# Optimization experiments

Hardware: AMD Instinct MI355X
Metric: run time of the kernel (lower is better)

The kernel has to match this reference:

```python
import jax, jax.numpy as jnp
import numpy as np

B, T, EPROJS, DUNITS, ATT_DIM, ODIM, LMAX = 16, 800, 512, 1024, 512, 5000, 96
SOS = EOS = ODIM - 1
SCALING = 2.0  # ESPnet AttAdd default softmax scaling


def setup_inputs() -> dict:
    key = jax.random.key(0)
    ks = jax.random.split(key, 16)
    w = lambda i, shape: (jax.random.normal(ks[i], shape, jnp.float32) * 0.02)
    return {
        "hs_pad": jax.random.normal(ks[0], (B, T, EPROJS), jnp.float32),
        "hlens": jnp.full((B,), T, dtype=jnp.int32),
        "ys_pad": jax.random.randint(ks[1], (B, LMAX), 0, ODIM - 2, dtype=jnp.int32),
        "embed": w(2, (ODIM, DUNITS)),
        # layer 0 LSTMCell: input = [embed ; att_context]
        "W_ih0": w(3, (4 * DUNITS, DUNITS + EPROJS)),
        "W_hh0": w(4, (4 * DUNITS, DUNITS)),
        "b_ih0": jnp.zeros((4 * DUNITS,), jnp.float32),
        "b_hh0": jnp.zeros((4 * DUNITS,), jnp.float32),
        # layer 1 LSTMCell
        "W_ih1": w(5, (4 * DUNITS, DUNITS)),
        "W_hh1": w(6, (4 * DUNITS, DUNITS)),
        "b_ih1": jnp.zeros((4 * DUNITS,), jnp.float32),
        "b_hh1": jnp.zeros((4 * DUNITS,), jnp.float32),
        # AttAdd (additive attention)
        "W_enc": w(7, (ATT_DIM, EPROJS)),
        "b_enc": jnp.zeros((ATT_DIM,), jnp.float32),
        "W_dec": w(8, (ATT_DIM, DUNITS)),
        "gvec": w(9, (ATT_DIM,)),
        # output projection (context_residual=False -> dunits -> odim)
        "W_out": w(10, (ODIM, DUNITS)),
        "b_out": jnp.zeros((ODIM,), jnp.float32),
    }


def _lstm_cell(x, h, c, W_ih, W_hh, b_ih, b_hh):
    g = x @ W_ih.T + b_ih + h @ W_hh.T + b_hh  # (B, 4D), torch gate order i,f,g,o
    i, f, gg, o = jnp.split(g, 4, axis=-1)
    c_new = jax.nn.sigmoid(f) * c + jax.nn.sigmoid(i) * jnp.tanh(gg)
    h_new = jax.nn.sigmoid(o) * jnp.tanh(c_new)
    return h_new, c_new


def reference(hs_pad, hlens, ys_pad, embed, W_ih0, W_hh0, b_ih0, b_hh0,
              W_ih1, W_hh1, b_ih1, b_hh1, W_enc, b_enc, W_dec, gvec,
              W_out, b_out):
    batch = ys_pad.shape[0]
    # ys_in = [sos; y], ys_out = [y; eos]  (all targets full length -> no ignore_id)
    sos_col = jnp.full((batch, 1), SOS, dtype=ys_pad.dtype)
    eos_col = jnp.full((batch, 1), EOS, dtype=ys_pad.dtype)
    ys_in = jnp.concatenate([sos_col, ys_pad], axis=1)   # (B, L+1)
    ys_out = jnp.concatenate([ys_pad, eos_col], axis=1)  # (B, L+1)
    olength = ys_out.shape[1]

    eys = embed[ys_in]  # (B, L+1, D)  dropout_emb is identity (p=0)

    # precompute encoder projection for additive attention (done once, as in ESPnet)
    pre_enc = jnp.einsum('bte,ae->bta', hs_pad, W_enc) + b_enc  # (B, T, ATT)
    mask = jnp.arange(hs_pad.shape[1])[None, :] < hlens[:, None]  # (B, T)

    z0 = jnp.zeros((batch, DUNITS), hs_pad.dtype)
    zeros = (z0, z0, z0, z0)  # z0, c0, z1, c1

    def step(carry, ey_t):
        z0, c0, z1, c1 = carry
        # AttAdd: e = gvec . tanh(W_enc h + W_dec z0)
        dec_proj = z0 @ W_dec.T  # (B, ATT)
        e = jnp.tanh(pre_enc + dec_proj[:, None, :]) @ gvec  # (B, T)
        e = jnp.where(mask, e, -jnp.inf)
        att_w = jax.nn.softmax(SCALING * e, axis=-1)
        att_c = jnp.einsum('bt,bte->be', att_w, hs_pad)  # (B, EPROJS)
        x = jnp.concatenate([ey_t, att_c], axis=-1)  # (B, D+EPROJS)
        z0, c0 = _lstm_cell(x, z0, c0, W_ih0, W_hh0, b_ih0, b_hh0)
        z1, c1 = _lstm_cell(z0, z1, c1, W_ih1, W_hh1, b_ih1, b_hh1)
        return (z0, c0, z1, c1), z1

    _, z_all = jax.lax.scan(step, zeros, jnp.swapaxes(eys, 0, 1))  # (L+1, B, D)
    z_all = jnp.swapaxes(z_all, 0, 1)  # (B, L+1, D)

    logits = jnp.einsum('bld,od->blo', z_all, W_out) + b_out  # (B, L+1, ODIM)
    logp = jax.nn.log_softmax(logits, axis=-1)
    nll = -jnp.take_along_axis(logp, ys_out[..., None].astype(jnp.int32), axis=-1)[..., 0]
    loss = jnp.mean(nll)  # reduction='mean' over all tokens (no ignored targets)
    # ESPnet: self.loss *= (mean(len(ys_in)) - 1) = LMAX
    loss = loss * jnp.asarray(LMAX, loss.dtype)
    return loss
```

## Files before the change

kernel.cpp:

```cpp
#include <hip/hip_runtime.h>
#include <stdint.h>

#define Bsz 16
#define Tlen 800
#define EPROJS 512
#define DUNITS 1024
#define ATT 512
#define ODIM 5000
#define LMAX 96
#define OL 97
#define NTOK (OL*Bsz)
#define G4 (4*DUNITS)
#define KX 1536
#define KA1 2048
#define SOS_ID (ODIM-1)
#define NWG 512
#define TCH 25

typedef unsigned short u16;
typedef unsigned int u32;
typedef unsigned long long u64;
typedef short bfrag8 __attribute__((ext_vector_type(8)));
typedef float f32x4 __attribute__((ext_vector_type(4)));

__device__ __forceinline__ float bf2f(u16 u){
  union { uint32_t u; float f; } v; v.u = ((uint32_t)u) << 16; return v.f;
}
__device__ __forceinline__ u16 f2bf(float f){
  union { float f; uint32_t u; } v; v.f = f;
  uint32_t r = v.u + 0x7FFFu + ((v.u >> 16) & 1u);
  return (u16)(r >> 16);
}
__device__ __forceinline__ float sigm(float x){ return 1.0f/(1.0f + __expf(-x)); }
__device__ __forceinline__ float tanh_f(float x){ return 1.0f - 2.0f/(__expf(2.0f*x) + 1.0f); }

__device__ __forceinline__ u64 ald64(const void* p){
  return __hip_atomic_load((const u64*)p, __ATOMIC_RELAXED, __HIP_MEMORY_SCOPE_AGENT);
}
__device__ __forceinline__ void ast64(void* p, u64 v){
  __hip_atomic_store((u64*)p, v, __ATOMIC_RELAXED, __HIP_MEMORY_SCOPE_AGENT);
}
__device__ __forceinline__ float aldf(const float* p){
  return __hip_atomic_load(p, __ATOMIC_RELAXED, __HIP_MEMORY_SCOPE_AGENT);
}
__device__ __forceinline__ void astf(float* p, float v){
  __hip_atomic_store(p, v, __ATOMIC_RELAXED, __HIP_MEMORY_SCOPE_AGENT);
}
__device__ __forceinline__ void ast32(u32* p, u32 v){
  __hip_atomic_store(p, v, __ATOMIC_RELAXED, __HIP_MEMORY_SCOPE_AGENT);
}
__device__ __forceinline__ int ald32(const int* p){
  return __hip_atomic_load(p, __ATOMIC_RELAXED, __HIP_MEMORY_SCOPE_AGENT);
}
__device__ __forceinline__ bfrag8 aldfrag(const u16* p){
  union { u64 q[2]; bfrag8 f; } u;
  u.q[0] = ald64(p);
  u.q[1] = ald64(p + 4);
  return u.f;
}

__device__ __forceinline__ f32x4 mfma_loop_a(const u16* A, int lda,
                                             const u16* Bm, int ldb,
                                             int K, f32x4 acc){
  int lane = threadIdx.x & 63;
  const u16* pa = A + (size_t)(lane & 15) * lda + ((lane >> 4) * 8);
  const u16* pb = Bm + (size_t)(lane & 15) * ldb + ((lane >> 4) * 8);
  #pragma unroll 4
  for (int k = 0; k < K; k += 32){
    bfrag8 av = aldfrag(pa + k);
    bfrag8 bv = *(const bfrag8*)(pb + k);
    acc = __builtin_amdgcn_mfma_f32_16x16x32_bf16(av, bv, acc, 0, 0, 0);
  }
  return acc;
}
__device__ __forceinline__ f32x4 mfma_loop(const u16* A, int lda,
                                           const u16* Bm, int ldb,
                                           int K, f32x4 acc){
  int lane = threadIdx.x & 63;
  const u16* pa = A + (size_t)(lane & 15) * lda + ((lane >> 4) * 8);
  const u16* pb = Bm + (size_t)(lane & 15) * ldb + ((lane >> 4) * 8);
  #pragma unroll 4
  for (int k = 0; k < K; k += 32){
    bfrag8 av = *(const bfrag8*)(pa + k);
    bfrag8 bv = *(const bfrag8*)(pb + k);
    acc = __builtin_amdgcn_mfma_f32_16x16x32_bf16(av, bv, acc, 0, 0, 0);
  }
  return acc;
}

__device__ __forceinline__ void wait_slots(const u64* s64, int n64, int tgt){
  __syncthreads();
  if (threadIdx.x < 64){
    int ln = threadIdx.x;
    bool d0 = (ln >= n64), d1 = (ln + 64 >= n64);
    for(;;){
      if (!d0){ u64 v = ald64(&s64[ln]);
        d0 = ((int)(u32)v >= tgt) && ((int)(u32)(v >> 32) >= tgt); }
      if (!d1){ u64 v = ald64(&s64[ln + 64]);
        d1 = ((int)(u32)v >= tgt) && ((int)(u32)(v >> 32) >= tgt); }
      if (__all(d0 && d1)) break;
      __builtin_amdgcn_s_sleep(1);
    }
  }
  __syncthreads();
}
__device__ __forceinline__ void signal_slot(int* slot, int val){
  __syncthreads();
  if (threadIdx.x == 0) ast32((u32*)slot, (u32)val);
}

__global__ __launch_bounds__(256) void k_zero(float* p, int n){
  int i = blockIdx.x*256 + threadIdx.x;
  if (i < n) p[i] = 0.f;
}
__global__ __launch_bounds__(256) void k_cvt(const float* src, u16* dst, int n){
  int i = blockIdx.x*256 + threadIdx.x, st = gridDim.x*256;
  for (; i < n; i += st) dst[i] = f2bf(src[i]);
}
__global__ __launch_bounds__(256) void k_build_wc0p(const float* Whh0, const float* Wih0, u16* out){
  int i = blockIdx.x*256+threadIdx.x, n = 256*16*KX, st = gridDim.x*256;
  for (; i<n; i+=st){
    int k = i % KX, ws = i / KX;
    int s = ws & 15, w2 = ws >> 4;
    int r = (s>>2)*1024 + 4*w2 + (s&3);
    float v = (k < 1024) ? Whh0[(size_t)r*1024 + k] : Wih0[(size_t)r*KX + k];
    out[i] = f2bf(v);
  }
}
__global__ __launch_bounds__(256) void k_build_wc1p(const float* Wih1, const float* Whh1, u16* out){
  int i = blockIdx.x*256+threadIdx.x, n = 256*16*KA1, st = gridDim.x*256;
  for (; i<n; i+=st){
    int k = i % KA1, ws = i / KA1;
    int s = ws & 15, w2 = ws >> 4;
    int r = (s>>2)*1024 + 4*w2 + (s&3);
    float v = (k < 1024) ? Wih1[(size_t)r*1024 + k] : Whh1[(size_t)r*1024 + (k-1024)];
    out[i] = f2bf(v);
  }
}
__global__ __launch_bounds__(256) void k_build_wih0p(const float* Wih0, u16* out){
  int i = blockIdx.x*256+threadIdx.x, n = 256*16*DUNITS, st = gridDim.x*256;
  for (; i<n; i+=st){
    int k = i % DUNITS, ws = i / DUNITS;
    int s = ws & 15, w2 = ws >> 4;
    int r = (s>>2)*1024 + 4*w2 + (s&3);
    out[i] = f2bf(Wih0[(size_t)r*KX + k]);
  }
}
__global__ __launch_bounds__(256) void k_build_aey(const float* embed, const int* ys_pad, u16* out){
  int i = blockIdx.x*256+threadIdx.x, n = NTOK*DUNITS, st = gridDim.x*256;
  for (; i<n; i+=st){
    int row = i / DUNITS, k = i % DUNITS;
    int l = row / Bsz, b = row % Bsz;
    int idx = (l == 0) ? SOS_ID : ys_pad[b*LMAX + (l-1)];
    out[i] = f2bf(embed[(size_t)idx*DUNITS + k]);
  }
}

__global__ __launch_bounds__(64) void k_gemm_preenc(const u16* hsb, const u16* Wenc,
                                                    const float* b_enc, u16* pre_enc){
  int bid = blockIdx.x;
  int m0 = (bid >> 5) * 16, n0 = (bid & 31) * 16;
  int lane = threadIdx.x & 63;
  int col = n0 + (lane & 15);
  float bias = b_enc[col];
  f32x4 acc = {bias, bias, bias, bias};
  acc = mfma_loop(hsb + (size_t)m0*EPROJS, EPROJS, Wenc + (size_t)n0*EPROJS, EPROJS, EPROJS, acc);
  int quad = lane >> 4;
  #pragma unroll
  for (int r = 0; r < 4; r++)
    pre_enc[(size_t)(m0 + quad*4 + r)*ATT + col] = f2bf(acc[r]);
}

__global__ __launch_bounds__(64) void k_gemm_logits(const u16* zall, const u16* Woutb,
                                                    const float* b_out, float* logits){
  const int NT = 313;
  int bid = blockIdx.x;
  int m0 = (bid / NT) * 16, n0 = (bid % NT) * 16;
  int lane = threadIdx.x & 63;
  int col = n0 + (lane & 15);
  bool ok = col < ODIM;
  int brow = ok ? col : 0;
  float bias = ok ? b_out[col] : 0.f;
  f32x4 acc = {bias, bias, bias, bias};
  const u16* pa = zall + (size_t)m0*DUNITS + (size_t)(lane & 15)*DUNITS + (lane >> 4)*8;
  const u16* pb = Woutb + (size_t)brow*DUNITS + (lane >> 4)*8;
  #pragma unroll 4
  for (int k = 0; k < DUNITS; k += 32){
    bfrag8 av = *(const bfrag8*)(pa + k);
    bfrag8 bv = *(const bfrag8*)(pb + k);
    acc = __builtin_amdgcn_mfma_f32_16x16x32_bf16(av, bv, acc, 0, 0, 0);
  }
  int quad = lane >> 4;
  if (ok){
    #pragma unroll
    for (int r = 0; r < 4; r++)
      logits[(size_t)(m0 + quad*4 + r)*ODIM + col] = acc[r];
  }
}

__global__ __launch_bounds__(256) void k_nll(const float* logits, const int* ys_pad, float* nll){
  int n = blockIdx.x;
  int b = n & 15, l = n >> 4;
  const float* row = logits + (size_t)n * ODIM;
  __shared__ float red[256];
  float m = -1e30f;
  for (int i = threadIdx.x; i < ODIM; i += 256) m = fmaxf(m, row[i]);
  red[threadIdx.x] = m; __syncthreads();
  for (int s = 128; s > 0; s >>= 1){
    if (threadIdx.x < s) red[threadIdx.x] = fmaxf(red[threadIdx.x], red[threadIdx.x + s]);
    __syncthreads();
  }
  float M = red[0]; __syncthreads();
  float sum = 0.f;
  for (int i = threadIdx.x; i < ODIM; i += 256) sum += __expf(row[i] - M);
  red[threadIdx.x] = sum; __syncthreads();
  for (int s = 128; s > 0; s >>= 1){
    if (threadIdx.x < s) red[threadIdx.x] += red[threadIdx.x + s];
    __syncthreads();
  }
  if (threadIdx.x == 0){
    int tgt = (l < LMAX) ? ys_pad[b*LMAX + l] : (ODIM - 1);
    nll[n] = (M + __logf(red[0])) - row[tgt];
  }
}

__global__ __launch_bounds__(256) void k_loss(const float* nll, float* out){
  __shared__ float red[256];
  float s = 0.f;
  for (int i = threadIdx.x; i < NTOK; i += 256) s += nll[i];
  red[threadIdx.x] = s; __syncthreads();
  for (int st = 128; st > 0; st >>= 1){
    if (threadIdx.x < st) red[threadIdx.x] += red[threadIdx.x + st];
    __syncthreads();
  }
  if (threadIdx.x == 0) out[0] = red[0] * ((float)LMAX / (float)NTOK);
}

__global__ __launch_bounds__(256, 2) void k_persist(
  const u16* __restrict__ peb, const u16* __restrict__ hsb,
  const u16* __restrict__ wc0p, const u16* __restrict__ wc1p, const u16* __restrict__ wdecb,
  const u16* __restrict__ wih0p, const u16* __restrict__ aey,
  const float* __restrict__ b_ih0, const float* __restrict__ b_hh0,
  const float* __restrict__ b_ih1, const float* __restrict__ b_hh1,
  const float* __restrict__ gvec, const int* __restrict__ hlens,
  u16* a1b0, u16* a1b1, float* dpbuf, float* part, float* partS, u16* xatt,
  u16* zall, int* bar)
{
  __shared__ __align__(16) u16 s_pe[TCH*512];
  __shared__ __align__(16) u16 s_hs[TCH*512];
  __shared__ __align__(16) float s_dp[512];
  __shared__ __align__(16) float s_gv[512];
  __shared__ __align__(16) float s_red[2048];
  __shared__ float s_c[64];
  __shared__ float s_bias[16];
  __shared__ float s_bias0[16];
  __shared__ float s_sp[4];
  __shared__ __align__(8) u16 s_h[64];

  int tid = threadIdx.x, blk = blockIdx.x;
  int wv = tid >> 6, ln = tid & 63;
  int s2_b = blk >> 5, s2_ch = blk & 31;
  int t0 = s2_ch * TCH;
  int hl = hlens[s2_b];
  bool isLow = (blk < 256);
  int hw = blk - 256;
  bool isdp = (!isLow) && ((hw & 7) == 0);
  int wdp = hw >> 3;

  int* z0s  = bar;
  int* z1s  = bar + 256;
  int* dps  = bar + 512;
  int* atts = bar + 544;
  int* parts= bar + 576;

  {
    const bfrag8* src_pe = (const bfrag8*)(peb + ((size_t)(s2_b*Tlen + t0))*512);
    const bfrag8* src_hs = (const bfrag8*)(hsb + ((size_t)(s2_b*Tlen + t0))*512);
    for (int idx = tid; idx < TCH*512/8; idx += 256){
      ((bfrag8*)s_pe)[idx] = src_pe[idx];
      ((bfrag8*)s_hs)[idx] = src_hs[idx];
    }
    for (int a = tid; a < 512; a += 256) s_gv[a] = gvec[a];
    if (isLow && tid < 16){
      int r = (tid>>2)*1024 + 4*blk + (tid&3);
      s_bias[tid] = b_ih1[r] + b_hh1[r];
    }
    if (!isLow && tid < 16){
      int r = (tid>>2)*1024 + 4*hw + (tid&3);
      s_bias0[tid] = b_ih0[r] + b_hh0[r];
    }
    if (tid < 64) s_c[tid] = 0.f;
  }
  __syncthreads();

  for (int i = 0; i < OL; i++){
    int par = i & 1;
    const u16* a1r = par ? a1b1 : a1b0;
    u16* a1w = par ? a1b0 : a1b1;
    float* dpc   = dpbuf + (size_t)par*(16*512);
    float* partc = part  + (size_t)par*(16*32*512);
    float* pSc   = partS + (size_t)par*(16*32);
    u16*   xac   = xatt  + (size_t)par*(16*512);

    f32x4 acc0 = {0.f,0.f,0.f,0.f};

    if (!isLow){
      if (isdp){
        if (i >= 1) wait_slots((const u64*)z0s, 128, i);
        const u16* btd = wdecb + (size_t)wdp*16*DUNITS;
        f32x4 ad = {0.f,0.f,0.f,0.f};
        ad = mfma_loop_a(a1r + wv*256, KA1, btd + wv*256, DUNITS, 256, ad);
        int q = ln >> 4;
        #pragma unroll
        for (int r = 0; r < 4; r++) s_red[wv*256 + (q*4+r)*16 + (ln & 15)] = ad[r];
        __syncthreads();
        {
          float val = s_red[tid] + s_red[256+tid] + s_red[512+tid] + s_red[768+tid];
          int b = tid >> 4, al = tid & 15;
          astf(&dpc[b*512 + wdp*16 + al], val);
        }
        signal_slot(&dps[wdp], i + 1);
      }
      acc0 = mfma_loop(aey + ((size_t)i*Bsz)*DUNITS + wv*256, DUNITS,
                       wih0p + (size_t)hw*16*DUNITS + wv*256, DUNITS, 256, acc0);
    }

    wait_slots((const u64*)dps, 16, i + 1);
    ((u64*)s_dp)[tid] = ald64(((const u64*)(dpc + s2_b*512)) + tid);
    __syncthreads();
    {
      float dpr[8], gvr[8];
      {
        float4 d1 = *(const float4*)&s_dp[ln*8];
        float4 d2 = *(const float4*)&s_dp[ln*8+4];
        float4 g1 = *(const float4*)&s_gv[ln*8];
        float4 g2 = *(const float4*)&s_gv[ln*8+4];
        dpr[0]=d1.x; dpr[1]=d1.y; dpr[2]=d1.z; dpr[3]=d1.w;
        dpr[4]=d2.x; dpr[5]=d2.y; dpr[6]=d2.z; dpr[7]=d2.w;
        gvr[0]=g1.x; gvr[1]=g1.y; gvr[2]=g1.z; gvr[3]=g1.w;
        gvr[4]=g2.x; gvr[5]=g2.y; gvr[6]=g2.z; gvr[7]=g2.w;
      }
      float attc[8];
      #pragma unroll
      for (int j = 0; j < 8; j++) attc[j] = 0.f;
      float sp = 0.f;
      for (int lt = wv; lt < TCH; lt += 4){
        int t = t0 + lt;
        bool valid = (t < hl);
        float e = 0.f;
        if (valid){
          bfrag8 pv = *(const bfrag8*)&s_pe[lt*512 + ln*8];
          #pragma unroll
          for (int j = 0; j < 8; j++){
            float x = bf2f(((u16*)&pv)[j]) + dpr[j];
            e += gvr[j] * tanh_f(x);
          }
        }
        #pragma unroll
        for (int off = 32; off > 0; off >>= 1) e += __shfl_xor(e, off, 64);
        float p = valid ? __expf(2.0f * e) : 0.f;
        if (ln == 0) sp += p;
        bfrag8 hv = *(const bfrag8*)&s_hs[lt*512 + ln*8];
        #pragma unroll
        for (int j = 0; j < 8; j++) attc[j] += p * bf2f(((u16*)&hv)[j]);
      }
      *(float4*)&s_red[wv*512 + ln*8]     = make_float4(attc[0],attc[1],attc[2],attc[3]);
      *(float4*)&s_red[wv*512 + ln*8 + 4] = make_float4(attc[4],attc[5],attc[6],attc[7]);
      if (ln == 0) s_sp[wv] = sp;
      __syncthreads();
      {
        int e0 = 2*tid;
        float v0 = s_red[e0]   + s_red[512+e0]   + s_red[1024+e0]   + s_red[1536+e0];
        float v1 = s_red[e0+1] + s_red[512+e0+1] + s_red[1024+e0+1] + s_red[1536+e0+1];
        union { float f[2]; u64 q; } pu; pu.f[0]=v0; pu.f[1]=v1;
        ast64(&partc[((size_t)(s2_b*32 + s2_ch))*512 + e0], pu.q);
      }
      if (tid == 0) astf(&pSc[s2_b*32 + s2_ch], s_sp[0]+s_sp[1]+s_sp[2]+s_sp[3]);
      signal_slot(&parts[s2_b*32 + s2_ch], i + 1);
    }

    if (isLow){
      if (blk < 16 && wv == 0){
        const int* myparts = parts + blk*32;
        bool dn = (ln >= 32);
        for(;;){
          if (!dn) dn = (ald32(&myparts[ln]) >= i + 1);
          if (__all(dn)) break;
          __builtin_amdgcn_s_sleep(1);
        }
        float sp = (ln < 32) ? aldf(&pSc[blk*32 + ln]) : 0.f;
        #pragma unroll
        for (int off = 32; off > 0; off >>= 1) sp += __shfl_xor(sp, off, 64);
        float rinv = 1.0f / sp;
        float v0=0.f,v1=0.f,v2=0.f,v3=0.f,v4=0.f,v5=0.f,v6=0.f,v7=0.f;
        #pragma unroll 8
        for (int c2 = 0; c2 < 32; c2++){
          const u64* pp = (const u64*)(partc + ((size_t)(blk*32 + c2))*512) + ln*4;
          union { u64 q; float f[2]; } x0,x1,x2,x3;
          x0.q = ald64(pp); x1.q = ald64(pp+1);
          x2.q = ald64(pp+2); x3.q = ald64(pp+3);
          v0 += x0.f[0]; v1 += x0.f[1]; v2 += x1.f[0]; v3 += x1.f[1];
          v4 += x2.f[0]; v5 += x2.f[1]; v6 += x3.f[0]; v7 += x3.f[1];
        }
        u32 p0 = (u32)f2bf(v0*rinv) | ((u32)f2bf(v1*rinv) << 16);
        u32 p1 = (u32)f2bf(v2*rinv) | ((u32)f2bf(v3*rinv) << 16);
        u32 p2 = (u32)f2bf(v4*rinv) | ((u32)f2bf(v5*rinv) << 16);
        u32 p3 = (u32)f2bf(v6*rinv) | ((u32)f2bf(v7*rinv) << 16);
        ast64(&xac[blk*512 + ln*8],     ((u64)p1 << 32) | p0);
        ast64(&xac[blk*512 + ln*8 + 4], ((u64)p3 << 32) | p2);
        asm volatile("s_waitcnt vmcnt(0)" ::: "memory");
        if (ln == 0) ast32((u32*)&atts[blk], (u32)(i + 1));
      }
      if (i >= 1){
        if (i >= 2) wait_slots((const u64*)z1s, 128, i);
        const u16* bt = wc1p + (size_t)blk*16*KA1;
        f32x4 acc = {0.f,0.f,0.f,0.f};
        acc = mfma_loop_a(a1r + wv*512, KA1, bt + wv*512, KA1, 512, acc);
        int q = ln >> 4;
        #pragma unroll
        for (int r = 0; r < 4; r++) s_red[wv*256 + (q*4+r)*16 + (ln & 15)] = acc[r];
        __syncthreads();
        {
          float val = s_red[tid] + s_red[256+tid] + s_red[512+tid] + s_red[768+tid]
                    + s_bias[tid & 15];
          s_red[1024 + tid] = val;
        }
        __syncthreads();
        if (tid < 64){
          int b = tid >> 2, jj = tid & 3;
          float gi = s_red[1024 + b*16 + jj];
          float gf = s_red[1024 + b*16 + 4 + jj];
          float gg = s_red[1024 + b*16 + 8 + jj];
          float go = s_red[1024 + b*16 + 12 + jj];
          float c = s_c[tid];
          float cn = sigm(gf)*c + sigm(gi)*tanh_f(gg);
          float h  = sigm(go)*tanh_f(cn);
          s_c[tid] = cn;
          s_h[tid] = f2bf(h);
        }
        __syncthreads();
        if (tid < 16){
          u64 hq = ((u64*)s_h)[tid];
          ast64(&a1w[tid*KA1 + 1024 + 4*blk], hq);
          *(u64*)&zall[((size_t)(i-1)*Bsz + tid)*DUNITS + 4*blk] = hq;
        }
        signal_slot(&z1s[blk], i + 1);
      }
    } else {
      const u16* bt0 = wc0p + (size_t)hw*16*KX;
      acc0 = mfma_loop_a(a1r + wv*256, KA1, bt0 + wv*256, KX, 256, acc0);
      wait_slots((const u64*)atts, 8, i + 1);
      acc0 = mfma_loop_a(xac + wv*128, 512, bt0 + 1024 + wv*128, KX, 128, acc0);
      int q = ln >> 4;
      #pragma unroll
      for (int r = 0; r < 4; r++) s_red[wv*256 + (q*4+r)*16 + (ln & 15)] = acc0[r];
      __syncthreads();
      {
        float val = s_red[tid] + s_red[256+tid] + s_red[512+tid] + s_red[768+tid]
                  + s_bias0[tid & 15];
        s_red[1024 + tid] = val;
      }
      __syncthreads();
      if (tid < 64){
        int b = tid >> 2, jj = tid & 3;
        float gi = s_red[1024 + b*16 + jj];
        float gf = s_red[1024 + b*16 + 4 + jj];
        float gg = s_red[1024 + b*16 + 8 + jj];
        float go = s_red[1024 + b*16 + 12 + jj];
        float c = s_c[tid];
        float cn = sigm(gf)*c + sigm(gi)*tanh_f(gg);
        float h  = sigm(go)*tanh_f(cn);
        s_c[tid] = cn;
        s_h[tid] = f2bf(h);
      }
      __syncthreads();
      if (tid < 16) ast64(&a1w[tid*KA1 + 4*hw], ((u64*)s_h)[tid]);
      signal_slot(&z0s[hw], i + 1);
    }
  }

  if (isLow){
    wait_slots((const u64*)z0s, 128, OL);
    wait_slots((const u64*)z1s, 128, OL);
    const u16* a1r = (OL & 1) ? a1b1 : a1b0;
    const u16* bt = wc1p + (size_t)blk*16*KA1;
    f32x4 acc = {0.f,0.f,0.f,0.f};
    acc = mfma_loop_a(a1r + wv*512, KA1, bt + wv*512, KA1, 512, acc);
    int q = ln >> 4;
    #pragma unroll
    for (int r = 0; r < 4; r++) s_red[wv*256 + (q*4+r)*16 + (ln & 15)] = acc[r];
    __syncthreads();
    {
      float val = s_red[tid] + s_red[256+tid] + s_red[512+tid] + s_red[768+tid]
                + s_bias[tid & 15];
      s_red[1024 + tid] = val;
    }
    __syncthreads();
    if (tid < 64){
      int b = tid >> 2, jj = tid & 3;
      float gi = s_red[1024 + b*16 + jj];
      float gf = s_red[1024 + b*16 + 4 + jj];
      float gg = s_red[1024 + b*16 + 8 + jj];
      float go = s_red[1024 + b*16 + 12 + jj];
      float c = s_c[tid];
      float cn = sigm(gf)*c + sigm(gi)*tanh_f(gg);
      float h  = sigm(go)*tanh_f(cn);
      s_h[tid] = f2bf(h);
    }
    __syncthreads();
    if (tid < 16)
      *(u64*)&zall[((size_t)LMAX*Bsz + tid)*DUNITS + 4*blk] = ((u64*)s_h)[tid];
  }
}

extern "C" void kernel_launch(void* const* d_in, const int* in_sizes, int n_in,
                              void* d_out, int out_size, void* d_ws, size_t ws_size,
                              hipStream_t stream)
{
  const float* hs     = (const float*)d_in[0];
  const int*   hlens  = (const int*)d_in[1];
  const int*   ys_pad = (const int*)d_in[2];
  const float* embed  = (const float*)d_in[3];
  const float* W_ih0  = (const float*)d_in[4];
  const float* W_hh0  = (const float*)d_in[5];
  const float* b_ih0  = (const float*)d_in[6];
  const float* b_hh0  = (const float*)d_in[7];
  const float* W_ih1  = (const float*)d_in[8];
  const float* W_hh1  = (const float*)d_in[9];
  const float* b_ih1  = (const float*)d_in[10];
  const float* b_hh1  = (const float*)d_in[11];
  const float* W_enc  = (const float*)d_in[12];
  const float* b_enc  = (const float*)d_in[13];
  const float* W_dec  = (const float*)d_in[14];
  const float* gvec   = (const float*)d_in[15];
  const float* W_out  = (const float*)d_in[16];
  const float* b_out  = (const float*)d_in[17];
  (void)in_sizes; (void)n_in; (void)out_size; (void)ws_size;

  char* w = (char*)d_ws;
  size_t off = 0;
  auto alloc = [&](size_t bytes)->char*{
    char* ptr = w + off;
    off += (bytes + 255) & ~(size_t)255;
    return ptr;
  };
  int*   bar  = (int*)alloc(8192);
  u16*  a1b0  = (u16*)alloc(Bsz*KA1*2);
  u16*  a1b1  = (u16*)alloc(Bsz*KA1*2);
  size_t state_bytes = off;
  float* dpbuf = (float*)alloc(2*(size_t)Bsz*ATT*4);
  float* part  = (float*)alloc(2*(size_t)Bsz*32*512*4);
  float* partS = (float*)alloc(2*(size_t)Bsz*32*4);
  u16*  xatt   = (u16*)alloc(2*(size_t)Bsz*512*2);
  u16*  hsb    = (u16*)alloc((size_t)Bsz*Tlen*EPROJS*2);
  u16*  peb    = (u16*)alloc((size_t)Bsz*Tlen*ATT*2);
  u16*  wencb  = (u16*)alloc((size_t)ATT*EPROJS*2);
  u16*  wdecb  = (u16*)alloc((size_t)ATT*DUNITS*2);
  u16*  wc0p   = (u16*)alloc((size_t)G4*KX*2);
  u16*  wc1p   = (u16*)alloc((size_t)G4*KA1*2);
  u16*  wih0p  = (u16*)alloc((size_t)G4*DUNITS*2);
  u16*  woutb  = (u16*)alloc((size_t)ODIM*DUNITS*2);
  u16*  aey    = (u16*)alloc((size_t)NTOK*DUNITS*2);
  u16*  zall   = (u16*)alloc((size_t)NTOK*DUNITS*2);
  float* logits= (float*)alloc((size_t)NTOK*ODIM*4);
  float* nll   = (float*)alloc(NTOK*4);

  {
    int n = (int)(state_bytes / 4);
    k_zero<<<(n + 255)/256, 256, 0, stream>>>((float*)w, n);
  }

  k_cvt<<<2048,256,0,stream>>>(hs, hsb, Bsz*Tlen*EPROJS);
  k_cvt<<<256,256,0,stream>>>(W_enc, wencb, ATT*EPROJS);
  k_cvt<<<512,256,0,stream>>>(W_dec, wdecb, ATT*DUNITS);
  k_cvt<<<2048,256,0,stream>>>(W_out, woutb, ODIM*DUNITS);
  k_build_wc0p<<<4096,256,0,stream>>>(W_hh0, W_ih0, wc0p);
  k_build_wc1p<<<4096,256,0,stream>>>(W_ih1, W_hh1, wc1p);
  k_build_wih0p<<<4096,256,0,stream>>>(W_ih0, wih0p);
  k_build_aey<<<1024,256,0,stream>>>(embed, ys_pad, aey);

  k_gemm_preenc<<<(Bsz*Tlen/16)*(ATT/16), 64, 0, stream>>>(hsb, wencb, b_enc, peb);

  {
    void* args[] = {
      (void*)&peb, (void*)&hsb, (void*)&wc0p, (void*)&wc1p, (void*)&wdecb,
      (void*)&wih0p, (void*)&aey, (void*)&b_ih0, (void*)&b_hh0,
      (void*)&b_ih1, (void*)&b_hh1, (void*)&gvec, (void*)&hlens,
      (void*)&a1b0, (void*)&a1b1, (void*)&dpbuf, (void*)&part, (void*)&partS,
      (void*)&xatt, (void*)&zall, (void*)&bar
    };
    hipLaunchCooperativeKernel((const void*)k_persist, dim3(NWG), dim3(256),
                               args, 0, stream);
  }

  k_gemm_logits<<<OL*313, 64, 0, stream>>>(zall, woutb, b_out, logits);
  k_nll<<<NTOK,256,0,stream>>>(logits, ys_pad, nll);
  k_loss<<<1,256,0,stream>>>(nll, (float*)d_out);
}
```

Measured before the change: 3.357 ms.

## Replace per-block flag barriers with sharded atomic counters and last-arriver attention reduction

After: 3.624 ms. 8.0% more time.

```diff
diff --git a/kernel.cpp b/kernel.cpp
--- a/kernel.cpp
+++ b/kernel.cpp
@@ -88,25 +88,30 @@
   return acc;
 }
 
-__device__ __forceinline__ void wait_slots(const u64* s64, int n64, int tgt){
+__device__ __forceinline__ void wait_cnt1(const int* p, int tgt){
+  __syncthreads();
+  if (threadIdx.x == 0){
+    while (ald32(p) < tgt) __builtin_amdgcn_s_sleep(1);
+  }
+  __syncthreads();
+}
+__device__ __forceinline__ void wait_cnt8(const int* base, int tgt){
   __syncthreads();
   if (threadIdx.x < 64){
     int ln = threadIdx.x;
-    bool d0 = (ln >= n64), d1 = (ln + 64 >= n64);
+    bool d = (ln >= 8);
     for(;;){
-      if (!d0){ u64 v = ald64(&s64[ln]);
-        d0 = ((int)(u32)v >= tgt) && ((int)(u32)(v >> 32) >= tgt); }
-      if (!d1){ u64 v = ald64(&s64[ln + 64]);
-        d1 = ((int)(u32)v >= tgt) && ((int)(u32)(v >> 32) >= tgt); }
-      if (__all(d0 && d1)) break;
+      if (!d) d = (ald32(base + ln*32) >= tgt);
+      if (__all(d)) break;
       __builtin_amdgcn_s_sleep(1);
     }
   }
   __syncthreads();
 }
-__device__ __forceinline__ void signal_slot(int* slot, int val){
+__device__ __forceinline__ void cnt_add(int* p){
   __syncthreads();
-  if (threadIdx.x == 0) ast32((u32*)slot, (u32)val);
+  if (threadIdx.x == 0)
+    (void)__hip_atomic_fetch_add(p, 1, __ATOMIC_RELAXED, __HIP_MEMORY_SCOPE_AGENT);
 }
 
 __global__ __launch_bounds__(256) void k_zero(float* p, int n){
@@ -256,6 +261,7 @@
   __shared__ float s_bias0[16];
   __shared__ float s_sp[4];
   __shared__ __align__(8) u16 s_h[64];
+  __shared__ int s_elect;
 
   int tid = threadIdx.x, blk = blockIdx.x;
   int wv = tid >> 6, ln = tid & 63;
@@ -267,11 +273,11 @@
   bool isdp = (!isLow) && ((hw & 7) == 0);
   int wdp = hw >> 3;
 
-  int* z0s  = bar;
-  int* z1s  = bar + 256;
-  int* dps  = bar + 512;
-  int* atts = bar + 544;
-  int* parts= bar + 576;
+  int* cntz0  = bar;
+  int* cntdp  = bar + 256;
+  int* cntatt = bar + 288;
+  int* cntz1  = bar + 320;
+  int* partcnt= bar + 576;
 
   {
     const bfrag8* src_pe = (const bfrag8*)(peb + ((size_t)(s2_b*Tlen + t0))*512);
@@ -306,7 +312,7 @@
 
     if (!isLow){
       if (isdp){
-        if (i >= 1) wait_slots((const u64*)z0s, 128, i);
+        if (i >= 1) wait_cnt8(cntz0, i*32);
         const u16* btd = wdecb + (size_t)wdp*16*DUNITS;
         f32x4 ad = {0.f,0.f,0.f,0.f};
         ad = mfma_loop_a(a1r + wv*256, KA1, btd + wv*256, DUNITS, 256, ad);
@@ -319,13 +325,13 @@
           int b = tid >> 4, al = tid & 15;
           astf(&dpc[b*512 + wdp*16 + al], val);
         }
-        signal_slot(&dps[wdp], i + 1);
+        cnt_add(cntdp);
       }
       acc0 = mfma_loop(aey + ((size_t)i*Bsz)*DUNITS + wv*256, DUNITS,
                        wih0p + (size_t)hw*16*DUNITS + wv*256, DUNITS, 256, acc0);
     }
 
-    wait_slots((const u64*)dps, 16, i + 1);
+    wait_cnt1(cntdp, (i + 1)*32);
     ((u64*)s_dp)[tid] = ald64(((const u64*)(dpc + s2_b*512)) + tid);
     __syncthreads();
     {
@@ -376,43 +382,40 @@
         ast64(&partc[((size_t)(s2_b*32 + s2_ch))*512 + e0], pu.q);
       }
       if (tid == 0) astf(&pSc[s2_b*32 + s2_ch], s_sp[0]+s_sp[1]+s_sp[2]+s_sp[3]);
-      signal_slot(&parts[s2_b*32 + s2_ch], i + 1);
-    }
-
-    if (isLow){
-      if (blk < 16 && wv == 0){
-        const int* myparts = parts + blk*32;
-        bool dn = (ln >= 32);
-        for(;;){
-          if (!dn) dn = (ald32(&myparts[ln]) >= i + 1);
-          if (__all(dn)) break;
-          __builtin_amdgcn_s_sleep(1);
-        }
-        float sp = (ln < 32) ? aldf(&pSc[blk*32 + ln]) : 0.f;
+    }
+    __syncthreads();
+    if (tid == 0){
+      int old = __hip_atomic_fetch_add(&partcnt[s2_b], 1,
+                                       __ATOMIC_RELAXED, __HIP_MEMORY_SCOPE_AGENT);
+      s_elect = (old == i*32 + 31);
+    }
+    __syncthreads();
+    if (s_elect){
+      float v0 = 0.f, v1 = 0.f;
+      const u64* pp = (const u64*)(partc + ((size_t)s2_b*32)*512) + tid;
+      #pragma unroll 8
+      for (int c2 = 0; c2 < 32; c2++){
+        union { u64 q; float f[2]; } x; x.q = ald64(pp + (size_t)c2*256);
+        v0 += x.f[0]; v1 += x.f[1];
+      }
+      if (wv == 0){
+        float sp = (ln < 32) ? aldf(&pSc[s2_b*32 + ln]) : 0.f;
         #pragma unroll
         for (int off = 32; off > 0; off >>= 1) sp += __shfl_xor(sp, off, 64);
-        float rinv = 1.0f / sp;
-        float v0=0.f,v1=0.f,v2=0.f,v3=0.f,v4=0.f,v5=0.f,v6=0.f,v7=0.f;
-        #pragma unroll 8
-        for (int c2 = 0; c2 < 32; c2++){
-          const u64* pp = (const u64*)(partc + ((size_t)(blk*32 + c2))*512) + ln*4;
-          union { u64 q; float f[2]; } x0,x1,x2,x3;
-          x0.q = ald64(pp); x1.q = ald64(pp+1);
-          x2.q = ald64(pp+2); x3.q = ald64(pp+3);
-          v0 += x0.f[0]; v1 += x0.f[1]; v2 += x1.f[0]; v3 += x1.f[1];
-          v4 += x2.f[0]; v5 += x2.f[1]; v6 += x3.f[0]; v7 += x3.f[1];
-        }
-        u32 p0 = (u32)f2bf(v0*rinv) | ((u32)f2bf(v1*rinv) << 16);
-        u32 p1 = (u32)f2bf(v2*rinv) | ((u32)f2bf(v3*rinv) << 16);
-        u32 p2 = (u32)f2bf(v4*rinv) | ((u32)f2bf(v5*rinv) << 16);
-        u32 p3 = (u32)f2bf(v6*rinv) | ((u32)f2bf(v7*rinv) << 16);
-        ast64(&xac[blk*512 + ln*8],     ((u64)p1 << 32) | p0);
-        ast64(&xac[blk*512 + ln*8 + 4], ((u64)p3 << 32) | p2);
-        asm volatile("s_waitcnt vmcnt(0)" ::: "memory");
-        if (ln == 0) ast32((u32*)&atts[blk], (u32)(i + 1));
-      }
+        if (ln == 0) s_sp[0] = 1.0f / sp;
+      }
+      __syncthreads();
+      float rinv = s_sp[0];
+      u32 wpk = (u32)f2bf(v0*rinv) | ((u32)f2bf(v1*rinv) << 16);
+      ast32(((u32*)xac) + s2_b*256 + tid, wpk);
+      __syncthreads();
+      if (tid == 0)
+        (void)__hip_atomic_fetch_add(cntatt, 1, __ATOMIC_RELAXED, __HIP_MEMORY_SCOPE_AGENT);
+    }
+
+    if (isLow){
       if (i >= 1){
-        if (i >= 2) wait_slots((const u64*)z1s, 128, i);
+        if (i >= 2) wait_cnt8(cntz1, (i-1)*32);
         const u16* bt = wc1p + (size_t)blk*16*KA1;
         f32x4 acc = {0.f,0.f,0.f,0.f};
         acc = mfma_loop_a(a1r + wv*512, KA1, bt + wv*512, KA1, 512, acc);
@@ -444,12 +447,12 @@
           ast64(&a1w[tid*KA1 + 1024 + 4*blk], hq);
           *(u64*)&zall[((size_t)(i-1)*Bsz + tid)*DUNITS + 4*blk] = hq;
         }
-        signal_slot(&z1s[blk], i + 1);
+        cnt_add(cntz1 + (blk & 7)*32);
       }
     } else {
       const u16* bt0 = wc0p + (size_t)hw*16*KX;
       acc0 = mfma_loop_a(a1r + wv*256, KA1, bt0 + wv*256, KX, 256, acc0);
-      wait_slots((const u64*)atts, 8, i + 1);
+      wait_cnt1(cntatt, (i + 1)*16);
       acc0 = mfma_loop_a(xac + wv*128, 512, bt0 + 1024 + wv*128, KX, 128, acc0);
       int q = ln >> 4;
       #pragma unroll
@@ -475,13 +478,13 @@
       }
       __syncthreads();
       if (tid < 16) ast64(&a1w[tid*KA1 + 4*hw], ((u64*)s_h)[tid]);
-      signal_slot(&z0s[hw], i + 1);
+      cnt_add(cntz0 + (hw & 7)*32);
     }
   }
 
   if (isLow){
-    wait_slots((const u64*)z0s, 128, OL);
-    wait_slots((const u64*)z1s, 128, OL);
+    wait_cnt8(cntz0, OL*32);
+    wait_cnt8(cntz1, (OL-1)*32);
     const u16* a1r = (OL & 1) ? a1b1 : a1b0;
     const u16* bt = wc1p + (size_t)blk*16*KA1;
     f32x4 acc = {0.f,0.f,0.f,0.f};
```

## Narrow cross-block spin-waits and parallelize attention-context reduction across all waves

Applied to the files above, without the earlier changes.

Measured after the change: 3.288 ms. 2.1% less time.

```diff
diff --git a/kernel.cpp b/kernel.cpp
--- a/kernel.cpp
+++ b/kernel.cpp
@@ -306,7 +306,16 @@
 
     if (!isLow){
       if (isdp){
-        if (i >= 1) wait_slots((const u64*)z0s, 128, i);
+        if (i >= 1){
+          const u64* z64 = (const u64*)z0s;
+          bool d = (ln >= 32);
+          for(;;){
+            if (!d){ u64 v = ald64(&z64[wv*32 + ln]);
+              d = ((int)(u32)v >= i) && ((int)(u32)(v >> 32) >= i); }
+            if (__all(d)) break;
+            __builtin_amdgcn_s_sleep(1);
+          }
+        }
         const u16* btd = wdecb + (size_t)wdp*16*DUNITS;
         f32x4 ad = {0.f,0.f,0.f,0.f};
         ad = mfma_loop_a(a1r + wv*256, KA1, btd + wv*256, DUNITS, 256, ad);
@@ -380,39 +389,47 @@
     }
 
     if (isLow){
-      if (blk < 16 && wv == 0){
-        const int* myparts = parts + blk*32;
-        bool dn = (ln >= 32);
-        for(;;){
-          if (!dn) dn = (ald32(&myparts[ln]) >= i + 1);
-          if (__all(dn)) break;
-          __builtin_amdgcn_s_sleep(1);
-        }
-        float sp = (ln < 32) ? aldf(&pSc[blk*32 + ln]) : 0.f;
-        #pragma unroll
-        for (int off = 32; off > 0; off >>= 1) sp += __shfl_xor(sp, off, 64);
-        float rinv = 1.0f / sp;
-        float v0=0.f,v1=0.f,v2=0.f,v3=0.f,v4=0.f,v5=0.f,v6=0.f,v7=0.f;
+      if (blk < 16){
+        if (wv == 0){
+          const int* myparts = parts + blk*32;
+          bool dn = (ln >= 32);
+          for(;;){
+            if (!dn) dn = (ald32(&myparts[ln]) >= i + 1);
+            if (__all(dn)) break;
+            __builtin_amdgcn_s_sleep(1);
+          }
+        }
+        __syncthreads();
+        float v0 = 0.f, v1 = 0.f;
+        const u64* pp = (const u64*)(partc + ((size_t)blk*32)*512) + tid;
         #pragma unroll 8
         for (int c2 = 0; c2 < 32; c2++){
-          const u64* pp = (const u64*)(partc + ((size_t)(blk*32 + c2))*512) + ln*4;
-          union { u64 q; float f[2]; } x0,x1,x2,x3;
-          x0.q = ald64(pp); x1.q = ald64(pp+1);
-          x2.q = ald64(pp+2); x3.q = ald64(pp+3);
-          v0 += x0.f[0]; v1 += x0.f[1]; v2 += x1.f[0]; v3 += x1.f[1];
-          v4 += x2.f[0]; v5 += x2.f[1]; v6 += x3.f[0]; v7 += x3.f[1];
-        }
-        u32 p0 = (u32)f2bf(v0*rinv) | ((u32)f2bf(v1*rinv) << 16);
-        u32 p1 = (u32)f2bf(v2*rinv) | ((u32)f2bf(v3*rinv) << 16);
-        u32 p2 = (u32)f2bf(v4*rinv) | ((u32)f2bf(v5*rinv) << 16);
-        u32 p3 = (u32)f2bf(v6*rinv) | ((u32)f2bf(v7*rinv) << 16);
-        ast64(&xac[blk*512 + ln*8],     ((u64)p1 << 32) | p0);
-        ast64(&xac[blk*512 + ln*8 + 4], ((u64)p3 << 32) | p2);
-        asm volatile("s_waitcnt vmcnt(0)" ::: "memory");
-        if (ln == 0) ast32((u32*)&atts[blk], (u32)(i + 1));
+          union { u64 q; float f[2]; } x; x.q = ald64(pp + (size_t)c2*256);
+          v0 += x.f[0]; v1 += x.f[1];
+        }
+        if (wv == 0){
+          float sp = (ln < 32) ? aldf(&pSc[blk*32 + ln]) : 0.f;
+          #pragma unroll
+          for (int off = 32; off > 0; off >>= 1) sp += __shfl_xor(sp, off, 64);
+          if (ln == 0) s_sp[0] = 1.0f / sp;
+        }
+        __syncthreads();
+        float rinv = s_sp[0];
+        u32 wpk = (u32)f2bf(v0*rinv) | ((u32)f2bf(v1*rinv) << 16);
+        ast32(((u32*)xac) + blk*256 + tid, wpk);
+        signal_slot(&atts[blk], i + 1);
       }
       if (i >= 1){
-        if (i >= 2) wait_slots((const u64*)z1s, 128, i);
+        if (i >= 2 && wv >= 2){
+          const u64* z64 = (const u64*)z1s;
+          bool d = false;
+          for(;;){
+            if (!d){ u64 v = ald64(&z64[(wv-2)*64 + ln]);
+              d = ((int)(u32)v >= i) && ((int)(u32)(v >> 32) >= i); }
+            if (__all(d)) break;
+            __builtin_amdgcn_s_sleep(1);
+          }
+        }
         const u16* bt = wc1p + (size_t)blk*16*KA1;
         f32x4 acc = {0.f,0.f,0.f,0.f};
         acc = mfma_loop_a(a1r + wv*512, KA1, bt + wv*512, KA1, 512, acc);
@@ -438,13 +455,15 @@
           s_c[tid] = cn;
           s_h[tid] = f2bf(h);
         }
-        __syncthreads();
-        if (tid < 16){
-          u64 hq = ((u64*)s_h)[tid];
-          ast64(&a1w[tid*KA1 + 1024 + 4*blk], hq);
-          *(u64*)&zall[((size_t)(i-1)*Bsz + tid)*DUNITS + 4*blk] = hq;
-        }
-        signal_slot(&z1s[blk], i + 1);
+        if (wv == 0){
+          if (ln < 16){
+            u64 hq = ((u64*)s_h)[ln];
+            ast64(&a1w[ln*KA1 + 1024 + 4*blk], hq);
+            *(u64*)&zall[((size_t)(i-1)*Bsz + ln)*DUNITS + 4*blk] = hq;
+          }
+          asm volatile("s_waitcnt vmcnt(0)" ::: "memory");
+          if (ln == 0) ast32((u32*)&z1s[blk], (u32)(i + 1));
+        }
       }
     } else {
       const u16* bt0 = wc0p + (size_t)hw*16*KX;
@@ -473,9 +492,11 @@
         s_c[tid] = cn;
         s_h[tid] = f2bf(h);
       }
-      __syncthreads();
-      if (tid < 16) ast64(&a1w[tid*KA1 + 4*hw], ((u64*)s_h)[tid]);
-      signal_slot(&z0s[hw], i + 1);
+      if (wv == 0){
+        if (ln < 16) ast64(&a1w[ln*KA1 + 4*hw], ((u64*)s_h)[ln]);
+        asm volatile("s_waitcnt vmcnt(0)" ::: "memory");
+        if (ln == 0) ast32((u32*)&z0s[hw], (u32)(i + 1));
+      }
     }
   }
 
```
